# Kernel optimization log

Hardware: AMD Instinct MI355X
Metric: run time of the kernel (lower is better)

Reference implementation:

```python
import jax, jax.numpy as jnp
import numpy as np

N = 20000     # nodes
E = 640000    # edges (before self-loops)
IN = 256      # in_feats
H = 8         # heads
HF = 64       # h_feats (per-head hidden channels)
OUT = 32      # out_feats (per-head output channels)
NEG_SLOPE = 0.2  # PyG GATConv default


def setup_inputs() -> dict:
    key = jax.random.key(0)
    ks = jax.random.split(key, 10)
    s = 0.1
    return {
        "x": jax.random.normal(ks[0], (N, IN), jnp.float32),
        "edge_index": jax.random.randint(ks[1], (2, E), 0, N),
        "W1": jax.random.normal(ks[2], (IN, H * HF), jnp.float32) * s,
        "att_src1": jax.random.normal(ks[3], (H, HF), jnp.float32) * s,
        "att_dst1": jax.random.normal(ks[4], (H, HF), jnp.float32) * s,
        "b1": jax.random.normal(ks[5], (HF,), jnp.float32) * s,
        "W2": jax.random.normal(ks[6], (HF, H * OUT), jnp.float32) * s,
        "att_src2": jax.random.normal(ks[7], (H, OUT), jnp.float32) * s,
        "att_dst2": jax.random.normal(ks[8], (H, OUT), jnp.float32) * s,
        "b2": jax.random.normal(ks[9], (OUT,), jnp.float32) * s,
    }


def _gat_conv(x, src, dst, W, a_src, a_dst, b, heads, ch, n):
    # project: [n, heads, ch]
    h = (x @ W).reshape(n, heads, ch)
    # per-node attention logits [n, heads]
    asrc = jnp.einsum('nhc,hc->nh', h, a_src)
    adst = jnp.einsum('nhc,hc->nh', h, a_dst)
    # per-edge attention (message j(src) -> i(dst)): [E', heads]
    e = jax.nn.leaky_relu(asrc[src] + adst[dst], NEG_SLOPE)
    # softmax over incoming edges of each dst node (numerically stable)
    m = jax.ops.segment_max(e, dst, num_segments=n)
    ex = jnp.exp(e - m[dst])
    den = jax.ops.segment_sum(ex, dst, num_segments=n)
    alpha = ex / den[dst]
    # weighted scatter-aggregate of source features: [n, heads, ch]
    out = jax.ops.segment_sum(alpha[:, :, None] * h[src], dst, num_segments=n)
    # concat=False -> mean over heads, then bias
    return out.mean(axis=1) + b


def reference(x, edge_index, W1, att_src1, att_dst1, b1, W2, att_src2, att_dst2, b2):
    n = x.shape[0]
    # PyG GATConv adds self-loops by default
    loops = jnp.arange(n, dtype=edge_index.dtype)
    src = jnp.concatenate([edge_index[0], loops])
    dst = jnp.concatenate([edge_index[1], loops])
    # dropout p=0.6 is identity in eval mode
    h = jax.nn.relu(_gat_conv(x, src, dst, W1, att_src1, att_dst1, b1, H, HF, n))
    return _gat_conv(h, src, dst, W2, att_src2, att_dst2, b2, H, OUT, n)
```

## Files before the change

kernel.cpp:

```cpp
#include <hip/hip_runtime.h>
#include <hip/hip_fp16.h>

#define N_NODES 20000
#define E_EDGES 640000
#define BCAP 96

using half8_t = __attribute__((ext_vector_type(8))) _Float16;
using f32x4   = __attribute__((ext_vector_type(4))) float;

__device__ __forceinline__ void fma8(float acc[8], float w, const uint4& v) {
    const _Float16* hv = (const _Float16*)&v;
    #pragma unroll
    for (int c = 0; c < 8; ++c) acc[c] += w * (float)hv[c];
}

__global__ __launch_bounds__(256) void prep_w1t_kernel(const float* __restrict__ W1,
                                                       __half* __restrict__ W1t,
                                                       int* __restrict__ deg) {
    int idx = blockIdx.x * 256 + threadIdx.x;
    if (idx < 20000) deg[idx] = 0;
    if (idx >= 151072) return;
    if (idx >= 20000) {
        int t = idx - 20000;
        int nn = t >> 8, k = t & 255;
        W1t[t] = __float2half(W1[(size_t)k * 512 + nn]);
    }
}

__global__ __launch_bounds__(256) void gemm_scatter_prep_kernel(
        const float* __restrict__ A, const __half* __restrict__ Bt,
        __half* __restrict__ C,
        const float* __restrict__ att_src, const float* __restrict__ att_dst,
        float* __restrict__ asrc_o, float* __restrict__ adst_o, int M,
        const int* __restrict__ ei, int e, int n,
        int* __restrict__ deg, int* __restrict__ csr_b,
        const float* __restrict__ W2,
        const float* __restrict__ as2, const float* __restrict__ ad2,
        __half* __restrict__ W2f, float* __restrict__ uv) {
    constexpr int K = 256, N = 512, LDA = 264, LDB = 40;
    constexpr int GB = 626;
    constexpr int SB = 2579;
    __shared__ __align__(16) _Float16 As[64 * LDA];
    __shared__ __align__(16) _Float16 Bs[128 * LDB];
    const int bid = blockIdx.x;
    const int tid = threadIdx.x;

    if (bid >= GB && bid < GB + SB) {
        int i = (bid - GB) * 256 + tid;
        if (i >= e + n) return;
        int s, d;
        if (i < e) { s = ei[i]; d = ei[e + i]; }
        else       { s = i - e; d = s; }
        int slot = atomicAdd(&deg[d], 1);
        csr_b[(size_t)d * BCAP + slot] = s;
        return;
    }
    if (bid >= GB + SB) {
        int idx = (bid - GB - SB) * 256 + tid;
        if (idx < 16384) {
            int hk = idx & 511;
            int c = idx >> 9, h = hk >> 6, kk = hk & 63;
            W2f[idx] = __float2half(W2[(size_t)kk * 256 + h * 32 + c]);
        } else if (idx < 17408) {
            int t = idx - 16384;
            int which = t >> 9;
            int hh = (t & 511) >> 6, kk = t & 63;
            const float* a = which ? ad2 : as2;
            float s = 0.f;
            #pragma unroll
            for (int c = 0; c < 32; ++c)
                s += W2[(size_t)kk * 256 + hh * 32 + c] * a[hh * 32 + c];
            uv[t] = s;
        }
        return;
    }

    const int by = (bid >= 313) ? 1 : 0;
    const int bx = bid - by * 313;
    const int bm = bx * 64;
    const int w = tid >> 6;
    const int lane = tid & 63;
    const int l16 = lane & 15;
    const int quad = lane >> 4;

    {
        const int ar = tid >> 2;
        const int kq = (tid & 3) * 64;
        const int gr = bm + ar;
        #pragma unroll
        for (int kk = 0; kk < 64; kk += 4) {
            float4 av = make_float4(0.f, 0.f, 0.f, 0.f);
            if (gr < M) av = *(const float4*)&A[(size_t)gr * K + kq + kk];
            union { __half h[4]; uint2 u; } pk;
            pk.h[0] = __float2half(av.x); pk.h[1] = __float2half(av.y);
            pk.h[2] = __float2half(av.z); pk.h[3] = __float2half(av.w);
            *(uint2*)&As[ar * LDA + kq + kk] = pk.u;
        }
    }

    const int b_r = tid >> 2;
    const int b_k8 = (tid & 3) * 8;
    #pragma unroll
    for (int bn2 = 0; bn2 < 2; ++bn2) {
        const int bn = (by * 2 + bn2) * 128;
        f32x4 acc[8];
        #pragma unroll
        for (int c = 0; c < 8; ++c) acc[c] = (f32x4){0.f, 0.f, 0.f, 0.f};

        for (int k0 = 0; k0 < K; k0 += 32) {
            #pragma unroll
            for (int rr = 0; rr < 2; ++rr) {
                const int row = b_r + rr * 64;
                uint4 bv = *(const uint4*)&Bt[(size_t)(bn + row) * K + k0 + b_k8];
                *(uint4*)&Bs[row * LDB + b_k8] = bv;
            }
            __syncthreads();
            const half8_t af = *(const half8_t*)&As[(w * 16 + l16) * LDA + k0 + quad * 8];
            #pragma unroll
            for (int c = 0; c < 8; ++c) {
                const half8_t bf = *(const half8_t*)&Bs[(c * 16 + l16) * LDB + quad * 8];
                acc[c] = __builtin_amdgcn_mfma_f32_16x16x32_f16(af, bf, acc[c], 0, 0, 0);
            }
            __syncthreads();
        }

        #pragma unroll
        for (int c = 0; c < 8; ++c) {
            #pragma unroll
            for (int r = 0; r < 4; ++r) {
                int row = bm + w * 16 + quad * 4 + r;
                if (row < M)
                    C[(size_t)row * N + bn + c * 16 + l16] = __float2half(acc[c][r]);
            }
        }

        const int hb0 = (by * 2 + bn2) * 2;
        #pragma unroll
        for (int g = 0; g < 2; ++g) {
            float ps[4] = {0.f, 0.f, 0.f, 0.f}, pd[4] = {0.f, 0.f, 0.f, 0.f};
            #pragma unroll
            for (int cc = 0; cc < 4; ++cc) {
                const int c = g * 4 + cc;
                float av = att_src[(hb0 + g) * 64 + cc * 16 + l16];
                float dv = att_dst[(hb0 + g) * 64 + cc * 16 + l16];
                #pragma unroll
                for (int r = 0; r < 4; ++r) {
                    ps[r] += acc[c][r] * av;
                    pd[r] += acc[c][r] * dv;
                }
            }
            #pragma unroll
            for (int r = 0; r < 4; ++r) {
                #pragma unroll
                for (int off = 8; off; off >>= 1) {
                    ps[r] += __shfl_down(ps[r], off, 16);
                    pd[r] += __shfl_down(pd[r], off, 16);
                }
            }
            if (l16 == 0) {
                #pragma unroll
                for (int r = 0; r < 4; ++r) {
                    int row = bm + w * 16 + quad * 4 + r;
                    if (row < M) {
                        asrc_o[row * 8 + hb0 + g] = ps[r];
                        adst_o[row * 8 + hb0 + g] = pd[r];
                    }
                }
            }
        }
    }
}

__global__ __launch_bounds__(256) void aggregate1_kernel(const __half* __restrict__ h,
                                                         const float* __restrict__ asrc,
                                                         const float* __restrict__ adst,
                                                         const int* __restrict__ deg_arr,
                                                         const int* __restrict__ csr_b,
                                                         __half* __restrict__ partial) {
    constexpr int MAXD = 64;
    constexpr int LDE = 66;
    __shared__ __align__(16) uint2 s_oe[4][8 * LDE];
    const int head = blockIdx.x & 7;
    const int gg = blockIdx.x >> 3;
    const int wv = threadIdx.x >> 6;
    const int lane = threadIdx.x & 63;
    const int d = lane >> 3;
    const int il = lane & 7;
    const int i = (gg * 4 + wv) * 8 + d;
    const int start = i * BCAP;
    const int deg = deg_arr[i];
    const float ad = adst[i * 8 + head];
    const bool fast = (deg <= MAXD);

    float lsum = 0.f;
    for (int k = il; k < deg; k += 8) {
        int j = csr_b[start + k];
        float e = asrc[j * 8 + head] + ad;
        e = e > 0.f ? e : 0.2f * e;
        float ex = __expf(e);
        if (fast)
            s_oe[wv][d * LDE + k] = make_uint2((unsigned)(j * 1024), __float_as_uint(ex));
        lsum += ex;
    }
    lsum += __shfl_xor(lsum, 1, 64);
    lsum += __shfl_xor(lsum, 2, 64);
    lsum += __shfl_xor(lsum, 4, 64);
    const float dinv = 1.0f / lsum;

    const int c0 = il * 8;
    const char* __restrict__ hb = (const char*)h + (head * 64 + c0) * 2;
    float acc[8];
    #pragma unroll
    for (int c = 0; c < 8; ++c) acc[c] = 0.f;

    if (fast) {
        const uint2* __restrict__ row = &s_oe[wv][d * LDE];
        int k = 0;
        if (deg >= 8) {
            uint4 q0 = *(const uint4*)&row[0];
            uint4 q1 = *(const uint4*)&row[2];
            uint4 v0 = *(const uint4*)(hb + q0.x);
            uint4 v1 = *(const uint4*)(hb + q0.z);
            uint4 v2 = *(const uint4*)(hb + q1.x);
            uint4 v3 = *(const uint4*)(hb + q1.z);
            for (k = 4; k + 3 < deg; k += 4) {
                uint4 nq0 = *(const uint4*)&row[k];
                uint4 nq1 = *(const uint4*)&row[k + 2];
                uint4 nv0 = *(const uint4*)(hb + nq0.x);
                uint4 nv1 = *(const uint4*)(hb + nq0.z);
                uint4 nv2 = *(const uint4*)(hb + nq1.x);
                uint4 nv3 = *(const uint4*)(hb + nq1.z);
                fma8(acc, __uint_as_float(q0.y), v0);
                fma8(acc, __uint_as_float(q0.w), v1);
                fma8(acc, __uint_as_float(q1.y), v2);
                fma8(acc, __uint_as_float(q1.w), v3);
                q0 = nq0; q1 = nq1; v0 = nv0; v1 = nv1; v2 = nv2; v3 = nv3;
            }
            fma8(acc, __uint_as_float(q0.y), v0);
            fma8(acc, __uint_as_float(q0.w), v1);
            fma8(acc, __uint_as_float(q1.y), v2);
            fma8(acc, __uint_as_float(q1.w), v3);
        }
        for (; k < deg; ++k) {
            uint2 oe = row[k];
            uint4 v = *(const uint4*)(hb + oe.x);
            fma8(acc, __uint_as_float(oe.y), v);
        }
    } else {
        for (int k = 0; k < deg; ++k) {
            int j = csr_b[start + k];
            float e = asrc[j * 8 + head] + ad;
            e = e > 0.f ? e : 0.2f * e;
            uint4 v = *(const uint4*)(hb + (size_t)j * 1024);
            fma8(acc, __expf(e), v);
        }
    }

    union { __half h8[8]; uint4 u4; } pk;
    #pragma unroll
    for (int c = 0; c < 8; ++c) pk.h8[c] = __float2half(acc[c] * dinv);
    *(uint4*)&partial[((size_t)i * 8 + head) * 64 + c0] = pk.u4;
}

__global__ __launch_bounds__(256) void merge1_kernel(const __half* __restrict__ partial,
                                                     const float* __restrict__ bias,
                                                     const float* __restrict__ uv,
                                                     __half* __restrict__ y1,
                                                     float* __restrict__ asrc2,
                                                     float* __restrict__ adst2) {
    __shared__ float s_y[4][64];
    const int tid = threadIdx.x;
    const int wv = tid >> 6;
    const int c = tid & 63;
    const int i = blockIdx.x * 4 + wv;
    float s = 0.f;
    #pragma unroll
    for (int h8 = 0; h8 < 8; ++h8)
        s += __half2float(partial[((size_t)i * 8 + h8) * 64 + c]);
    s = s * 0.125f + bias[c];
    s = fmaxf(s, 0.f);
    y1[(size_t)i * 64 + c] = __float2half(s);
    s_y[wv][c] = s;
    const int t = c >> 2, cq = c & 3;
    const float* __restrict__ uvr = &uv[t * 64 + cq * 16];
    const float* __restrict__ sy = &s_y[wv][cq * 16];
    float dot = 0.f;
    #pragma unroll
    for (int m = 0; m < 16; ++m) dot += sy[m] * uvr[m];
    dot += __shfl_xor(dot, 1, 64);
    dot += __shfl_xor(dot, 2, 64);
    if (cq == 0) {
        if (t < 8) asrc2[i * 8 + t] = dot;
        else       adst2[i * 8 + (t - 8)] = dot;
    }
}

__global__ __launch_bounds__(256) void aggregate2_kernel(const __half* __restrict__ y1,
                                                         const float* __restrict__ asrc2,
                                                         const float* __restrict__ adst2,
                                                         const int* __restrict__ deg_arr,
                                                         const int* __restrict__ csr_b,
                                                         __half* __restrict__ S) {
    const int tid = threadIdx.x;
    const int wv = tid >> 6, lane = tid & 63;
    const int h = lane >> 3;
    const int c8 = (lane & 7) * 8;
    const int i = blockIdx.x * 4 + wv;
    const int start = i * BCAP;
    const int deg = deg_arr[i];
    const float adh = adst2[i * 8 + h];

    float acc[8];
    #pragma unroll
    for (int c = 0; c < 8; ++c) acc[c] = 0.f;
    float den = 0.f;

    auto step = [&](int j) {
        float e = asrc2[j * 8 + h] + adh;
        e = e > 0.f ? e : 0.2f * e;
        float ex = __expf(e);
        den += ex;
        uint4 yq = *(const uint4*)&y1[(size_t)j * 64 + c8];
        const _Float16* yv = (const _Float16*)&yq;
        #pragma unroll
        for (int c = 0; c < 8; ++c) acc[c] += ex * (float)yv[c];
    };

    int k = 0;
    uint4 jq = *(const uint4*)&csr_b[start];
    for (; k + 4 <= deg; k += 4) {
        uint4 jn = *(const uint4*)&csr_b[start + k + 4];
        step(jq.x); step(jq.y); step(jq.z); step(jq.w);
        jq = jn;
    }
    if (k < deg) { step(jq.x); ++k; }
    if (k < deg) { step(jq.y); ++k; }
    if (k < deg) { step(jq.z); ++k; }

    const float dinv = 1.0f / den;
    union { __half h8[8]; uint4 u4; } pk;
    #pragma unroll
    for (int c = 0; c < 8; ++c) pk.h8[c] = __float2half(acc[c] * dinv);
    *(uint4*)&S[(size_t)i * 512 + h * 64 + c8] = pk.u4;
}

__global__ __launch_bounds__(256) void gemm_out_kernel(const __half* __restrict__ A,
                                                       const __half* __restrict__ Bt,
                                                       const float* __restrict__ bias,
                                                       float* __restrict__ out, int M) {
    constexpr int K = 512, LD = 40;
    __shared__ __align__(16) _Float16 As[64 * LD];
    __shared__ __align__(16) _Float16 Bs[32 * LD];
    const int tid = threadIdx.x;
    const int bm = blockIdx.x * 64;
    const int w = tid >> 6, lane = tid & 63;
    const int l16 = lane & 15, quad = lane >> 4;
    f32x4 acc[2];
    #pragma unroll
    for (int c = 0; c < 2; ++c) acc[c] = (f32x4){0.f, 0.f, 0.f, 0.f};

    const int a_r = tid >> 2, a_k8 = (tid & 3) * 8;
    for (int k0 = 0; k0 < K; k0 += 32) {
        const int gr = bm + a_r;
        uint4 av = make_uint4(0, 0, 0, 0);
        if (gr < M) av = *(const uint4*)&A[(size_t)gr * K + k0 + a_k8];
        *(uint4*)&As[a_r * LD + a_k8] = av;
        if (tid < 128) {
            const int nr = tid >> 2, k8 = (tid & 3) * 8;
            *(uint4*)&Bs[nr * LD + k8] = *(const uint4*)&Bt[(size_t)nr * K + k0 + k8];
        }
        __syncthreads();
        const half8_t af = *(const half8_t*)&As[(w * 16 + l16) * LD + quad * 8];
        #pragma unroll
        for (int c = 0; c < 2; ++c) {
            const half8_t bf = *(const half8_t*)&Bs[(c * 16 + l16) * LD + quad * 8];
            acc[c] = __builtin_amdgcn_mfma_f32_16x16x32_f16(af, bf, acc[c], 0, 0, 0);
        }
        __syncthreads();
    }
    #pragma unroll
    for (int c = 0; c < 2; ++c) {
        #pragma unroll
        for (int r = 0; r < 4; ++r) {
            int row = bm + w * 16 + quad * 4 + r;
            if (row < M)
                out[(size_t)row * 32 + c * 16 + l16] =
                    acc[c][r] * 0.125f + bias[c * 16 + l16];
        }
    }
}

extern "C" void kernel_launch(void* const* d_in, const int* in_sizes, int n_in,
                              void* d_out, int out_size, void* d_ws, size_t ws_size,
                              hipStream_t stream) {
    const float* x   = (const float*)d_in[0];
    const int*   ei  = (const int*)d_in[1];
    const float* W1  = (const float*)d_in[2];
    const float* as1 = (const float*)d_in[3];
    const float* ad1 = (const float*)d_in[4];
    const float* b1  = (const float*)d_in[5];
    const float* W2  = (const float*)d_in[6];
    const float* as2 = (const float*)d_in[7];
    const float* ad2 = (const float*)d_in[8];
    const float* b2  = (const float*)d_in[9];

    const int n = N_NODES;
    const int e = E_EDGES;

    char* w = (char*)d_ws;
    __half* partial = (__half*)w; w += (size_t)n * 8 * 64 * 2;
    __half* h_buf   = (__half*)w; w += (size_t)n * 512 * 2;
    __half* y1h     = (__half*)w; w += (size_t)n * 64 * 2;
    __half* W1t     = (__half*)w; w += (size_t)512 * 256 * 2;
    __half* W2f     = (__half*)w; w += (size_t)32 * 512 * 2;
    float*  uv      = (float*)w;  w += (size_t)16 * 64 * 4;
    float*  asrc    = (float*)w;  w += (size_t)n * 8 * 4;
    float*  adst    = (float*)w;  w += (size_t)n * 8 * 4;
    int* deg        = (int*)w; w += (size_t)n * 4;
    int* csr_b      = (int*)w; w += (size_t)n * BCAP * 4;
    __half* S     = h_buf;
    float* asrc2  = asrc;
    float* adst2  = adst;

    prep_w1t_kernel<<<591, 256, 0, stream>>>(W1, W1t, deg);

    gemm_scatter_prep_kernel<<<626 + 2579 + 68, 256, 0, stream>>>(
        x, W1t, h_buf, as1, ad1, asrc, adst, n, ei, e, n, deg, csr_b,
        W2, as2, ad2, W2f, uv);

    aggregate1_kernel<<<(n / 32) * 8, 256, 0, stream>>>(h_buf, asrc, adst, deg,
                                                        csr_b, partial);
    merge1_kernel<<<n / 4, 256, 0, stream>>>(partial, b1, uv, y1h, asrc2, adst2);

    aggregate2_kernel<<<n / 4, 256, 0, stream>>>(y1h, asrc2, adst2, deg, csr_b, S);
    gemm_out_kernel<<<(n + 63) / 64, 256, 0, stream>>>(S, W2f, b2, (float*)d_out, n);
}
```

Before: 257.8 us.

## Store CSR indices as 16-bit and fuse aggregate2 with output GEMM

The CSR neighbour lists are now stored as unsigned 16-bit indices instead of 32-bit ints, which halves the index traffic in both aggregation kernels. Node ids up to 20000 fit in 16 bits. The second-layer aggregation is fused with the final 512x32 projection: each block stages W2f (32 KB) in XOR-swizzled shared memory and each wave computes one node's output row with scalar FMAs. This removes the S intermediate write/read and one launch, but every block reloads the 32 KB of weights, uses about 40 KB of LDS (which can cut occupancy), and replaces MFMA with scalar dot products.

```diff
diff --git a/kernel.cpp b/kernel.cpp
--- a/kernel.cpp
+++ b/kernel.cpp
@@ -33,7 +33,7 @@
         const float* __restrict__ att_src, const float* __restrict__ att_dst,
         float* __restrict__ asrc_o, float* __restrict__ adst_o, int M,
         const int* __restrict__ ei, int e, int n,
-        int* __restrict__ deg, int* __restrict__ csr_b,
+        int* __restrict__ deg, unsigned short* __restrict__ csr16,
         const float* __restrict__ W2,
         const float* __restrict__ as2, const float* __restrict__ ad2,
         __half* __restrict__ W2f, float* __restrict__ uv) {
@@ -52,7 +52,7 @@
         if (i < e) { s = ei[i]; d = ei[e + i]; }
         else       { s = i - e; d = s; }
         int slot = atomicAdd(&deg[d], 1);
-        csr_b[(size_t)d * BCAP + slot] = s;
+        csr16[(size_t)d * BCAP + slot] = (unsigned short)s;
         return;
     }
     if (bid >= GB + SB) {
@@ -175,7 +175,7 @@
                                                          const float* __restrict__ asrc,
                                                          const float* __restrict__ adst,
                                                          const int* __restrict__ deg_arr,
-                                                         const int* __restrict__ csr_b,
+                                                         const unsigned short* __restrict__ csr16,
                                                          __half* __restrict__ partial) {
     constexpr int MAXD = 64;
     constexpr int LDE = 66;
@@ -194,7 +194,7 @@
 
     float lsum = 0.f;
     for (int k = il; k < deg; k += 8) {
-        int j = csr_b[start + k];
+        int j = csr16[start + k];
         float e = asrc[j * 8 + head] + ad;
         e = e > 0.f ? e : 0.2f * e;
         float ex = __expf(e);
@@ -248,7 +248,7 @@
         }
     } else {
         for (int k = 0; k < deg; ++k) {
-            int j = csr_b[start + k];
+            int j = csr16[start + k];
             float e = asrc[j * 8 + head] + ad;
             e = e > 0.f ? e : 0.2f * e;
             uint4 v = *(const uint4*)(hb + (size_t)j * 1024);
@@ -295,13 +295,27 @@
     }
 }
 
-__global__ __launch_bounds__(256) void aggregate2_kernel(const __half* __restrict__ y1,
-                                                         const float* __restrict__ asrc2,
-                                                         const float* __restrict__ adst2,
-                                                         const int* __restrict__ deg_arr,
-                                                         const int* __restrict__ csr_b,
-                                                         __half* __restrict__ S) {
+__global__ __launch_bounds__(256) void aggregate2_out_kernel(
+        const __half* __restrict__ y1,
+        const float* __restrict__ asrc2, const float* __restrict__ adst2,
+        const int* __restrict__ deg_arr, const unsigned short* __restrict__ csr16,
+        const __half* __restrict__ W2f, const float* __restrict__ b2,
+        float* __restrict__ out) {
+    __shared__ __align__(16) _Float16 w2f_s[32 * 512];
+    __shared__ __align__(16) float s_row[4][512];
     const int tid = threadIdx.x;
+
+    {
+        const int o = tid >> 3, seg = tid & 7;
+        #pragma unroll
+        for (int q = 0; q < 8; ++q) {
+            int chunk = seg * 8 + q;
+            uint4 v = *(const uint4*)&W2f[o * 512 + chunk * 8];
+            *(uint4*)&w2f_s[o * 512 + ((chunk ^ (o & 7)) << 3)] = v;
+        }
+    }
+    __syncthreads();
+
     const int wv = tid >> 6, lane = tid & 63;
     const int h = lane >> 3;
     const int c8 = (lane & 7) * 8;
@@ -327,67 +341,42 @@
     };
 
     int k = 0;
-    uint4 jq = *(const uint4*)&csr_b[start];
+    uint2 jq = *(const uint2*)&csr16[start];
     for (; k + 4 <= deg; k += 4) {
-        uint4 jn = *(const uint4*)&csr_b[start + k + 4];
-        step(jq.x); step(jq.y); step(jq.z); step(jq.w);
+        uint2 jn = *(const uint2*)&csr16[start + k + 4];
+        step(jq.x & 0xffff); step(jq.x >> 16);
+        step(jq.y & 0xffff); step(jq.y >> 16);
         jq = jn;
     }
-    if (k < deg) { step(jq.x); ++k; }
-    if (k < deg) { step(jq.y); ++k; }
-    if (k < deg) { step(jq.z); ++k; }
+    if (k < deg) { step(jq.x & 0xffff); ++k; }
+    if (k < deg) { step(jq.x >> 16); ++k; }
+    if (k < deg) { step(jq.y & 0xffff); ++k; }
 
     const float dinv = 1.0f / den;
-    union { __half h8[8]; uint4 u4; } pk;
-    #pragma unroll
-    for (int c = 0; c < 8; ++c) pk.h8[c] = __float2half(acc[c] * dinv);
-    *(uint4*)&S[(size_t)i * 512 + h * 64 + c8] = pk.u4;
-}
-
-__global__ __launch_bounds__(256) void gemm_out_kernel(const __half* __restrict__ A,
-                                                       const __half* __restrict__ Bt,
-                                                       const float* __restrict__ bias,
-                                                       float* __restrict__ out, int M) {
-    constexpr int K = 512, LD = 40;
-    __shared__ __align__(16) _Float16 As[64 * LD];
-    __shared__ __align__(16) _Float16 Bs[32 * LD];
-    const int tid = threadIdx.x;
-    const int bm = blockIdx.x * 64;
-    const int w = tid >> 6, lane = tid & 63;
-    const int l16 = lane & 15, quad = lane >> 4;
-    f32x4 acc[2];
-    #pragma unroll
-    for (int c = 0; c < 2; ++c) acc[c] = (f32x4){0.f, 0.f, 0.f, 0.f};
-
-    const int a_r = tid >> 2, a_k8 = (tid & 3) * 8;
-    for (int k0 = 0; k0 < K; k0 += 32) {
-        const int gr = bm + a_r;
-        uint4 av = make_uint4(0, 0, 0, 0);
-        if (gr < M) av = *(const uint4*)&A[(size_t)gr * K + k0 + a_k8];
-        *(uint4*)&As[a_r * LD + a_k8] = av;
-        if (tid < 128) {
-            const int nr = tid >> 2, k8 = (tid & 3) * 8;
-            *(uint4*)&Bs[nr * LD + k8] = *(const uint4*)&Bt[(size_t)nr * K + k0 + k8];
-        }
-        __syncthreads();
-        const half8_t af = *(const half8_t*)&As[(w * 16 + l16) * LD + quad * 8];
-        #pragma unroll
-        for (int c = 0; c < 2; ++c) {
-            const half8_t bf = *(const half8_t*)&Bs[(c * 16 + l16) * LD + quad * 8];
-            acc[c] = __builtin_amdgcn_mfma_f32_16x16x32_f16(af, bf, acc[c], 0, 0, 0);
-        }
-        __syncthreads();
-    }
-    #pragma unroll
-    for (int c = 0; c < 2; ++c) {
-        #pragma unroll
-        for (int r = 0; r < 4; ++r) {
-            int row = bm + w * 16 + quad * 4 + r;
-            if (row < M)
-                out[(size_t)row * 32 + c * 16 + l16] =
-                    acc[c][r] * 0.125f + bias[c * 16 + l16];
-        }
-    }
+    {
+        f32x4 v0 = {acc[0] * dinv, acc[1] * dinv, acc[2] * dinv, acc[3] * dinv};
+        f32x4 v1 = {acc[4] * dinv, acc[5] * dinv, acc[6] * dinv, acc[7] * dinv};
+        *(f32x4*)&s_row[wv][h * 64 + c8] = v0;
+        *(f32x4*)&s_row[wv][h * 64 + c8 + 4] = v1;
+    }
+
+    const int o = lane & 31, part = lane >> 5;
+    float dot = 0.f;
+    #pragma unroll
+    for (int cc = 0; cc < 32; ++cc) {
+        const int chunk = part * 32 + cc;
+        uint4 wq = *(const uint4*)&w2f_s[o * 512 + ((chunk ^ (o & 7)) << 3)];
+        const _Float16* wh = (const _Float16*)&wq;
+        f32x4 s0 = *(const f32x4*)&s_row[wv][chunk * 8];
+        f32x4 s1 = *(const f32x4*)&s_row[wv][chunk * 8 + 4];
+        dot += s0[0] * (float)wh[0] + s0[1] * (float)wh[1] +
+               s0[2] * (float)wh[2] + s0[3] * (float)wh[3] +
+               s1[0] * (float)wh[4] + s1[1] * (float)wh[5] +
+               s1[2] * (float)wh[6] + s1[3] * (float)wh[7];
+    }
+    dot += __shfl_xor(dot, 32, 64);
+    if (part == 0)
+        out[(size_t)i * 32 + o] = dot * 0.125f + b2[o];
 }
 
 extern "C" void kernel_launch(void* const* d_in, const int* in_sizes, int n_in,
@@ -417,21 +406,21 @@
     float*  asrc    = (float*)w;  w += (size_t)n * 8 * 4;
     float*  adst    = (float*)w;  w += (size_t)n * 8 * 4;
     int* deg        = (int*)w; w += (size_t)n * 4;
-    int* csr_b      = (int*)w; w += (size_t)n * BCAP * 4;
-    __half* S     = h_buf;
+    unsigned short* csr16 = (unsigned short*)w;
+    w += (size_t)n * BCAP * 2 + 16;
     float* asrc2  = asrc;
     float* adst2  = adst;
 
     prep_w1t_kernel<<<591, 256, 0, stream>>>(W1, W1t, deg);
 
     gemm_scatter_prep_kernel<<<626 + 2579 + 68, 256, 0, stream>>>(
-        x, W1t, h_buf, as1, ad1, asrc, adst, n, ei, e, n, deg, csr_b,
+        x, W1t, h_buf, as1, ad1, asrc, adst, n, ei, e, n, deg, csr16,
         W2, as2, ad2, W2f, uv);
 
     aggregate1_kernel<<<(n / 32) * 8, 256, 0, stream>>>(h_buf, asrc, adst, deg,
-                                                        csr_b, partial);
+                                                        csr16, partial);
     merge1_kernel<<<n / 4, 256, 0, stream>>>(partial, b1, uv, y1h, asrc2, adst2);
 
-    aggregate2_kernel<<<n / 4, 256, 0, stream>>>(y1h, asrc2, adst2, deg, csr_b, S);
-    gemm_out_kernel<<<(n + 63) / 64, 256, 0, stream>>>(S, W2f, b2, (float*)d_out, n);
-}
+    aggregate2_out_kernel<<<n / 4, 256, 0, stream>>>(y1h, asrc2, adst2, deg, csr16,
+                                                     W2f, b2, (float*)d_out);
+}
```

Result: slower. 267.6 us (+3.8%).
